# Kernel optimization log

Measured on AMD Instinct MI355X. Metric: run time of the kernel, lower is better.

The kernel has to match this reference:

```python
import jax, jax.numpy as jnp
import numpy as np

D = 256
H = 4
DH = D // H
DFF = 1024
EPS = 1e-5


def _split_heads(x):
    B, L, _ = x.shape
    return x.reshape(B, L, H, DH).transpose(0, 2, 1, 3)  # [B,H,L,dh]


def _merge_heads(o):
    B, h, L, dh = o.shape
    return o.transpose(0, 2, 1, 3).reshape(B, L, h * dh)


def _attention(Q, K, V, M):
    # Q,K,V: [B,H,Lq/Lk,dh]; M: [B,Lq,Lk] or [B,1,Lk]
    A = jnp.einsum('bhqd,bhkd->bhqk', Q, K) / (DH ** 0.5)
    A = jnp.where(M[:, None] == 0, -jnp.inf, A)
    A = jax.nn.softmax(A, axis=-1)
    return jnp.einsum('bhqk,bhkd->bhqd', A, V)


def _layernorm(x, g, b):
    mu = jnp.mean(x, axis=-1, keepdims=True)
    var = jnp.mean(jnp.square(x - mu), axis=-1, keepdims=True)
    return (x - mu) * jax.lax.rsqrt(var + EPS) * g + b


def setup_inputs() -> dict:
    key = jax.random.key(0)
    ks = jax.random.split(key, 14)
    B, T, S = 16, 1024, 1024
    s = 1.0 / (D ** 0.5)
    inp = {
        'X_target': jax.random.normal(ks[0], (B, T, D), jnp.float32),
        'outputMask': jnp.ones((B, T), jnp.float32),
        'X_encoder': jax.random.normal(ks[1], (B, S, D), jnp.float32),
        'inputMask': jnp.ones((B, S), jnp.float32),
        'Wq1': jax.random.normal(ks[2], (D, D), jnp.float32) * s,
        'Wk1': jax.random.normal(ks[3], (D, D), jnp.float32) * s,
        'Wv1': jax.random.normal(ks[4], (D, D), jnp.float32) * s,
        'Wo1': jax.random.normal(ks[5], (D, D), jnp.float32) * s,
        'Wq2': jax.random.normal(ks[6], (D, D), jnp.float32) * s,
        'Wk2': jax.random.normal(ks[7], (D, D), jnp.float32) * s,
        'Wv2': jax.random.normal(ks[8], (D, D), jnp.float32) * s,
        'Wo2': jax.random.normal(ks[9], (D, D), jnp.float32) * s,
        'W1': jax.random.normal(ks[10], (DFF, D), jnp.float32) * s,
        'W2': jax.random.normal(ks[11], (D, DFF), jnp.float32) * (1.0 / (DFF ** 0.5)),
        'g1': jnp.ones((D,), jnp.float32), 'b1': jnp.zeros((D,), jnp.float32),
        'g2': jnp.ones((D,), jnp.float32), 'b2': jnp.zeros((D,), jnp.float32),
        'g3': jnp.ones((D,), jnp.float32), 'b3': jnp.zeros((D,), jnp.float32),
    }
    return inp


def reference(X_target, outputMask, X_encoder, inputMask,
              Wq1, Wk1, Wv1, Wo1, Wq2, Wk2, Wv2, Wo2,
              W1, W2, g1, b1, g2, b2, g3, b3):
    T = X_target.shape[1]
    # combined causal * padding mask (intended tril of ones)
    tril = jnp.tril(jnp.ones((T, T), X_target.dtype))
    M_self = outputMask[:, None, :] * tril  # [B,T,T]
    M_cross = inputMask[:, None, :]         # [B,1,S]

    # masked self-attention (Linear: x @ W.T)
    Q = _split_heads(X_target @ Wq1.T)
    K = _split_heads(X_target @ Wk1.T)
    V = _split_heads(X_target @ Wv1.T)
    O = _merge_heads(_attention(Q, K, V, M_self)) @ Wo1.T
    X = X_target + _layernorm(O, g1, b1)  # AddNorm (dropout eval=identity)

    # cross-attention; note: output proj is O @ Wo2 (no transpose) in source
    Q = _split_heads(X @ Wq2.T)
    K = _split_heads(X_encoder @ Wk2.T)
    V = _split_heads(X_encoder @ Wv2.T)
    O = _merge_heads(_attention(Q, K, V, M_cross)) @ Wo2
    X = X + _layernorm(O, g2, b2)

    # FFN with ReLU after both linears (as in source)
    F = jax.nn.relu(jax.nn.relu(X @ W1.T) @ W2.T)
    X = X + _layernorm(F, g3, b3)
    return X
```

## Files before the change

### kernel.cpp

```cpp
#include <hip/hip_runtime.h>
#include <math.h>

#define D_ 256
#define H_ 4
#define DH_ 64
#define NKT_ 16
#define TPB_BITS 10

typedef __attribute__((ext_vector_type(8))) short bf16x8;
typedef __attribute__((ext_vector_type(4))) short short4v;
typedef __attribute__((ext_vector_type(4))) float f32x4;

__device__ __forceinline__ short f2bf(float x) {
  union { float f; unsigned u; } c; c.f = x;
  unsigned r = (c.u + 0x7fffu + ((c.u >> 16) & 1u)) >> 16;
  return (short)r;
}
__device__ __forceinline__ float bf2f(short s) {
  union { unsigned u; float f; } c; c.u = ((unsigned)(unsigned short)s) << 16;
  return c.f;
}
__device__ __forceinline__ unsigned cvtpk(float lo, float hi) {
  unsigned r;
  asm("v_cvt_pk_bf16_f32 %0, %1, %2" : "=v"(r) : "v"(lo), "v"(hi));
  return r;
}
#if __has_builtin(__builtin_amdgcn_exp2f)
#define EXP2F(x) __builtin_amdgcn_exp2f(x)
#else
#define EXP2F(x) __expf(0.6931471805599453f * (x))
#endif

__device__ __forceinline__ void gl_lds16(const void* g, void* lds) {
  __builtin_amdgcn_global_load_lds((const __attribute__((address_space(1))) void*)g,
                                   (__attribute__((address_space(3))) void*)lds,
                                   16, 0, 0);
}

template<bool ABF16, bool TRANSB, bool RELU, bool CBF16>
__global__ __launch_bounds__(256) void gemm_mfma(
    const void* __restrict__ A0, const void* __restrict__ A1, const void* __restrict__ A2,
    const float* __restrict__ B0, const float* __restrict__ B1, const float* __restrict__ B2,
    void* __restrict__ C0, void* __restrict__ C1, void* __restrict__ C2,
    int N, int K, int M, int vtrans_z, int ktile_z) {
  __shared__ short Al[2][128][72];
  __shared__ short Bl[2][128][72];
  const int tid = threadIdx.x;
  const int w   = tid >> 6;
  const int l   = tid & 63;
  const int bn  = blockIdx.x * 128;
  const int bm  = blockIdx.y * 128;
  const int z   = blockIdx.z;
  const void*  Av = (z == 0) ? A0 : ((z == 1) ? A1 : A2);
  const float* B  = (z == 0) ? B0 : ((z == 1) ? B1 : B2);
  void*        Cv = (z == 0) ? C0 : ((z == 1) ? C1 : C2);
  const int wm = (w >> 1) * 64;
  const int wn = (w & 1) * 64;
  const int fr = l & 15;
  const int fg = l >> 4;

  f32x4 acc[4][4];
  #pragma unroll
  for (int mi = 0; mi < 4; ++mi)
    #pragma unroll
    for (int ni = 0; ni < 4; ++ni) acc[mi][ni] = (f32x4){0.f, 0.f, 0.f, 0.f};

  const int sr = tid >> 1;
  const int sc = (tid & 1) * 32;

  float4 arf[8]; bf16x8 arb[4]; float4 brf[8];

  auto loadA = [&](int k0) {
    if (ABF16) {
      const short* arow = (const short*)Av + (size_t)(bn + sr) * K + k0 + sc;
      #pragma unroll
      for (int i = 0; i < 4; ++i) arb[i] = *(const bf16x8*)&arow[i * 8];
    } else {
      const float* arow = (const float*)Av + (size_t)(bn + sr) * K + k0 + sc;
      #pragma unroll
      for (int i = 0; i < 8; ++i) arf[i] = *(const float4*)&arow[i * 4];
    }
  };
  auto loadB = [&](int k0) {
    if (TRANSB) {
      const float* brow = B + (size_t)(bm + sr) * K + k0 + sc;
      #pragma unroll
      for (int i = 0; i < 8; ++i) brf[i] = *(const float4*)&brow[i * 4];
    } else {
      #pragma unroll
      for (int i = 0; i < 8; ++i) {
        int idx = tid + i * 256;
        int kk = idx >> 5;
        int c4 = (idx & 31) * 4;
        brf[i] = *(const float4*)&B[(size_t)(k0 + kk) * M + bm + c4];
      }
    }
  };
  auto store = [&](int buf) {
    if (ABF16) {
      #pragma unroll
      for (int i = 0; i < 4; ++i) *(bf16x8*)&Al[buf][sr][sc + i * 8] = arb[i];
    } else {
      #pragma unroll
      for (int i = 0; i < 8; ++i) {
        float4 v = arf[i];
        short4v s; s[0] = f2bf(v.x); s[1] = f2bf(v.y); s[2] = f2bf(v.z); s[3] = f2bf(v.w);
        *(short4v*)&Al[buf][sr][sc + i * 4] = s;
      }
    }
    if (TRANSB) {
      #pragma unroll
      for (int i = 0; i < 8; ++i) {
        float4 v = brf[i];
        short4v s; s[0] = f2bf(v.x); s[1] = f2bf(v.y); s[2] = f2bf(v.z); s[3] = f2bf(v.w);
        *(short4v*)&Bl[buf][sr][sc + i * 4] = s;
      }
    } else {
      #pragma unroll
      for (int i = 0; i < 8; ++i) {
        int idx = tid + i * 256;
        int kk = idx >> 5;
        int c4 = (idx & 31) * 4;
        float4 v = brf[i];
        Bl[buf][c4 + 0][kk] = f2bf(v.x);
        Bl[buf][c4 + 1][kk] = f2bf(v.y);
        Bl[buf][c4 + 2][kk] = f2bf(v.z);
        Bl[buf][c4 + 3][kk] = f2bf(v.w);
      }
    }
  };

  loadA(0); loadB(0); store(0);
  __syncthreads();
  const int nk = K >> 6;
  for (int s = 0; s < nk; ++s) {
    const int cur = s & 1;
    if (s + 1 < nk) { loadA((s + 1) << 6); loadB((s + 1) << 6); }
    #pragma unroll
    for (int kh = 0; kh < 2; ++kh) {
      bf16x8 af[4], bfr[4];
      #pragma unroll
      for (int mi = 0; mi < 4; ++mi)
        af[mi] = *(bf16x8*)&Al[cur][wm + mi * 16 + fr][kh * 32 + fg * 8];
      #pragma unroll
      for (int ni = 0; ni < 4; ++ni)
        bfr[ni] = *(bf16x8*)&Bl[cur][wn + ni * 16 + fr][kh * 32 + fg * 8];
      #pragma unroll
      for (int mi = 0; mi < 4; ++mi)
        #pragma unroll
        for (int ni = 0; ni < 4; ++ni)
          acc[mi][ni] = __builtin_amdgcn_mfma_f32_16x16x32_bf16(af[mi], bfr[ni], acc[mi][ni], 0, 0, 0);
    }
    if (s + 1 < nk) store(cur ^ 1);
    __syncthreads();
  }

  if (z == vtrans_z) {
    #pragma unroll
    for (int mi = 0; mi < 4; ++mi) {
      int nbase = bn + wm + mi * 16 + fg * 4;
      int b_  = nbase >> TPB_BITS;
      int key = nbase & ((1 << TPB_BITS) - 1);
      int kt  = key >> 6, kin = key & 63;
      #pragma unroll
      for (int ni = 0; ni < 4; ++ni) {
        int col = bm + wn + ni * 16 + fr;
        int h_ = col >> 6, dh = col & 63;
        short4v s;
        #pragma unroll
        for (int reg = 0; reg < 4; ++reg) s[reg] = f2bf(acc[mi][ni][reg]);
        size_t off = ((((size_t)(b_ * H_ + h_) * NKT_) + kt) << 12)
                   + dh * 64 + (((kin >> 3) ^ (dh & 7)) << 3) + (kin & 7);
        *(short4v*)&((short*)Cv)[off] = s;
      }
    }
  } else if (z == ktile_z) {
    #pragma unroll
    for (int mi = 0; mi < 4; ++mi) {
      #pragma unroll
      for (int reg = 0; reg < 4; ++reg) {
        int tok = bn + wm + mi * 16 + fg * 4 + reg;
        int b_  = tok >> TPB_BITS;
        int key = tok & ((1 << TPB_BITS) - 1);
        int kt  = key >> 6, kin = key & 63;
        size_t tb = ((((size_t)(b_ * H_) * NKT_) + kt) << 12) + kin * 64;
        #pragma unroll
        for (int ni = 0; ni < 4; ++ni) {
          int col = bm + wn + ni * 16 + fr;
          int h_ = col >> 6, dh = col & 63;
          size_t off = tb + (((size_t)h_ * NKT_) << 12)
                     + (((dh >> 3) ^ (kin & 7)) << 3) + (dh & 7);
          ((short*)Cv)[off] = f2bf(acc[mi][ni][reg]);
        }
      }
    }
  } else {
    #pragma unroll
    for (int mi = 0; mi < 4; ++mi) {
      #pragma unroll
      for (int reg = 0; reg < 4; ++reg) {
        size_t rowbase = (size_t)(bn + wm + mi * 16 + fg * 4 + reg) * M + bm + wn;
        #pragma unroll
        for (int ni = 0; ni < 4; ++ni) {
          float v = acc[mi][ni][reg];
          if (RELU) v = fmaxf(v, 0.f);
          if (CBF16) ((short*)Cv)[rowbase + ni * 16 + fr] = f2bf(v);
          else       ((float*)Cv)[rowbase + ni * 16 + fr] = v;
        }
      }
    }
  }
}

template<bool CAUSAL>
__global__ __launch_bounds__(256) void attn_mfma(const short* __restrict__ Q,
                                                 const short* __restrict__ KT,
                                                 const short* __restrict__ VT,
                                                 const float* __restrict__ mask,
                                                 short* __restrict__ O,
                                                 int T, int Lk) {
  constexpr int NS = CAUSAL ? 2 : 1;
  __shared__ short Kl[2][64][64];
  __shared__ short Vl[2][64][64];
  __shared__ short Pl[4][16][64];
  const int tid = threadIdx.x;
  const int l   = tid & 63;
  const int w   = tid >> 6;
  const int bh  = blockIdx.x;
  const int b   = bh >> 2;
  const int h   = bh & 3;
  const int r   = l & 15;
  const int g   = l >> 4;
  const float SCL2E = 0.125f * 1.4426950408889634f;

  const short* Ktile = KT + (((size_t)bh * (Lk >> 6)) << 12);
  const short* Vtile = VT + (((size_t)bh * (Lk >> 6)) << 12);
  const float* mrow  = mask + (size_t)b * Lk;

  int qt[NS];
  qt[0] = blockIdx.y;
  if (CAUSAL) qt[NS - 1] = (T >> 6) - 1 - blockIdx.y;
  const int nkt = CAUSAL ? (qt[NS - 1] + 1) : (Lk >> 6);

  bf16x8 qf[NS][2];
  #pragma unroll
  for (int s = 0; s < NS; ++s) {
    const short* qrow = Q + ((size_t)(b * T + qt[s] * 64 + w * 16 + r)) * D_ + h * DH_;
    qf[s][0] = *(const bf16x8*)&qrow[g * 8];
    qf[s][1] = *(const bf16x8*)&qrow[32 + g * 8];
  }

  float m[NS], ls[NS];
  f32x4 acc[NS][4];
  #pragma unroll
  for (int s = 0; s < NS; ++s) {
    m[s] = -1e30f; ls[s] = 0.f;
    #pragma unroll
    for (int dt = 0; dt < 4; ++dt) acc[s][dt] = (f32x4){0.f, 0.f, 0.f, 0.f};
  }

  auto stage = [&](int kt, int bb) {
    const short* ks = Ktile + ((size_t)kt << 12) + w * 1024 + (size_t)l * 8;
    const short* vs = Vtile + ((size_t)kt << 12) + w * 1024 + (size_t)l * 8;
    char* kd = (char*)&Kl[bb][0][0] + w * 2048;
    char* vd = (char*)&Vl[bb][0][0] + w * 2048;
    gl_lds16(ks,       kd);
    gl_lds16(ks + 512, kd + 1024);
    gl_lds16(vs,       vd);
    gl_lds16(vs + 512, vd + 1024);
  };

  stage(0, 0);
  __syncthreads();

  const int rx = r & 7;
  for (int kt = 0; kt < nkt; ++kt) {
    const int buf = kt & 1;
    if (kt + 1 < nkt) stage(kt + 1, buf ^ 1);

    const char* kb = (const char*)&Kl[buf][0][0];
    const char* vb = (const char*)&Vl[buf][0][0];

    f32x4 sfr[NS][4];
    #pragma unroll
    for (int s = 0; s < NS; ++s)
      #pragma unroll
      for (int st = 0; st < 4; ++st) sfr[s][st] = (f32x4){0.f, 0.f, 0.f, 0.f};
    __builtin_amdgcn_s_setprio(1);
    #pragma unroll
    for (int st = 0; st < 4; ++st) {
      #pragma unroll
      for (int kh = 0; kh < 2; ++kh) {
        bf16x8 kf = *(const bf16x8*)(kb + (st * 16 + r) * 128 + (((kh * 4 + g) ^ rx) << 4));
        #pragma unroll
        for (int s = 0; s < NS; ++s)
          if (!CAUSAL || kt <= qt[s])
            sfr[s][st] = __builtin_amdgcn_mfma_f32_16x16x32_bf16(kf, qf[s][kh], sfr[s][st], 0, 0, 0);
      }
    }
    __builtin_amdgcn_s_setprio(0);

    float mb[4][4];
    #pragma unroll
    for (int st = 0; st < 4; ++st) {
      float4 mv = *(const float4*)&mrow[kt * 64 + st * 16 + g * 4];
      #pragma unroll
      for (int reg = 0; reg < 4; ++reg)
        mb[st][reg] = fmaf((&mv.x)[reg], 1e30f, -1e30f);
    }

    #pragma unroll
    for (int s = 0; s < NS; ++s) {
      if (CAUSAL && kt > qt[s]) continue;
      float sc[4][4];
      #pragma unroll
      for (int st = 0; st < 4; ++st)
        #pragma unroll
        for (int reg = 0; reg < 4; ++reg)
          sc[st][reg] = fmaf(sfr[s][st][reg], SCL2E, mb[st][reg]);
      if (CAUSAL && kt == qt[s]) {
        #pragma unroll
        for (int st = 0; st < 4; ++st)
          #pragma unroll
          for (int reg = 0; reg < 4; ++reg)
            if (st * 16 + g * 4 + reg > w * 16 + r) sc[st][reg] = -1e30f;
      }

      float tm = sc[0][0];
      #pragma unroll
      for (int st = 0; st < 4; ++st)
        #pragma unroll
        for (int reg = 0; reg < 4; ++reg) tm = fmaxf(tm, sc[st][reg]);
      tm = fmaxf(tm, __shfl_xor(tm, 16));
      tm = fmaxf(tm, __shfl_xor(tm, 32));
      const int need = __any(tm - m[s] > 8.f);
      float mnew = need ? fmaxf(m[s], tm) : m[s];
      float pe[4][4], psum = 0.f;
      #pragma unroll
      for (int st = 0; st < 4; ++st)
        #pragma unroll
        for (int reg = 0; reg < 4; ++reg) {
          pe[st][reg] = EXP2F(sc[st][reg] - mnew);
          psum += pe[st][reg];
        }
      psum += __shfl_xor(psum, 16);
      psum += __shfl_xor(psum, 32);
      char* pw = (char*)&Pl[w][0][0] + r * 128;
      #pragma unroll
      for (int st = 0; st < 4; ++st) {
        uint2 u;
        u.x = cvtpk(pe[st][0], pe[st][1]);
        u.y = cvtpk(pe[st][2], pe[st][3]);
        *(uint2*)(pw + (((st * 2 + (g >> 1)) ^ rx) << 4) + (g & 1) * 8) = u;
      }
      if (need) {
        float alpha = EXP2F(m[s] - mnew);
        ls[s] = ls[s] * alpha + psum;
        m[s] = mnew;
        float af[4];
        #pragma unroll
        for (int reg = 0; reg < 4; ++reg) af[reg] = __shfl(alpha, g * 4 + reg);
        #pragma unroll
        for (int dt = 0; dt < 4; ++dt)
          #pragma unroll
          for (int reg = 0; reg < 4; ++reg) acc[s][dt][reg] *= af[reg];
      } else {
        ls[s] += psum;
      }

      __builtin_amdgcn_s_setprio(1);
      #pragma unroll
      for (int kh = 0; kh < 2; ++kh) {
        bf16x8 pf = *(const bf16x8*)((const char*)&Pl[w][0][0] + r * 128 + (((kh * 4 + g) ^ rx) << 4));
        #pragma unroll
        for (int dt = 0; dt < 4; ++dt) {
          bf16x8 vf = *(const bf16x8*)(vb + (dt * 16 + r) * 128 + (((kh * 4 + g) ^ rx) << 4));
          acc[s][dt] = __builtin_amdgcn_mfma_f32_16x16x32_bf16(pf, vf, acc[s][dt], 0, 0, 0);
        }
      }
      __builtin_amdgcn_s_setprio(0);
    }

    __syncthreads();
  }

  #pragma unroll
  for (int s = 0; s < NS; ++s) {
    float inv = (ls[s] > 0.f) ? (1.f / ls[s]) : 0.f;
    float invf[4];
    #pragma unroll
    for (int reg = 0; reg < 4; ++reg) invf[reg] = __shfl(inv, g * 4 + reg);
    #pragma unroll
    for (int reg = 0; reg < 4; ++reg) {
      short* orow = O + ((size_t)(b * T + qt[s] * 64 + w * 16 + g * 4 + reg)) * D_ + h * DH_;
      #pragma unroll
      for (int dt = 0; dt < 4; ++dt)
        orow[dt * 16 + r] = f2bf(acc[s][dt][reg] * invf[reg]);
    }
  }
}

template<bool RBF16, bool OBF16>
__global__ __launch_bounds__(256) void ln_res(const short* __restrict__ F,
                                              const void* __restrict__ Rv,
                                              const float* __restrict__ g,
                                              const float* __restrict__ bt,
                                              void* __restrict__ outv) {
  const int lane = threadIdx.x & 63;
  const int wid  = threadIdx.x >> 6;
  const size_t row  = (size_t)blockIdx.x * 4 + wid;
  const size_t base = row * 256 + (size_t)lane * 4;
  short4v fv = *(const short4v*)&F[base];
  float vx = bf2f(fv[0]), vy = bf2f(fv[1]), vz = bf2f(fv[2]), vw = bf2f(fv[3]);
  float s = vx + vy + vz + vw;
  #pragma unroll
  for (int o = 32; o >= 1; o >>= 1) s += __shfl_xor(s, o);
  float mu = s * (1.f / 256.f);
  float dx = vx - mu, dy = vy - mu, dz = vz - mu, dw = vw - mu;
  float vr = dx * dx + dy * dy + dz * dz + dw * dw;
  #pragma unroll
  for (int o = 32; o >= 1; o >>= 1) vr += __shfl_xor(vr, o);
  float rstd = rsqrtf(vr * (1.f / 256.f) + 1e-5f);
  float4 g4 = *(const float4*)&g[lane * 4];
  float4 b4 = *(const float4*)&bt[lane * 4];
  float rx, ry, rz, rw;
  if (RBF16) {
    short4v r4 = *(const short4v*)&((const short*)Rv)[base];
    rx = bf2f(r4[0]); ry = bf2f(r4[1]); rz = bf2f(r4[2]); rw = bf2f(r4[3]);
  } else {
    float4 r4 = *(const float4*)&((const float*)Rv)[base];
    rx = r4.x; ry = r4.y; rz = r4.z; rw = r4.w;
  }
  float ox = fmaf(dx * rstd, g4.x, b4.x) + rx;
  float oy = fmaf(dy * rstd, g4.y, b4.y) + ry;
  float oz = fmaf(dz * rstd, g4.z, b4.z) + rz;
  float ow = fmaf(dw * rstd, g4.w, b4.w) + rw;
  if (OBF16) {
    uint2 u; u.x = cvtpk(ox, oy); u.y = cvtpk(oz, ow);
    *(uint2*)&((short*)outv)[base] = u;
  } else {
    *(float4*)&((float*)outv)[base] = make_float4(ox, oy, oz, ow);
  }
}

extern "C" void kernel_launch(void* const* d_in, const int* in_sizes, int n_in,
                              void* d_out, int out_size, void* d_ws, size_t ws_size,
                              hipStream_t stream) {
  const float* Xt    = (const float*)d_in[0];
  const float* oMask = (const float*)d_in[1];
  const float* Xe    = (const float*)d_in[2];
  const float* iMask = (const float*)d_in[3];
  const float* Wq1   = (const float*)d_in[4];
  const float* Wk1   = (const float*)d_in[5];
  const float* Wv1   = (const float*)d_in[6];
  const float* Wo1   = (const float*)d_in[7];
  const float* Wq2   = (const float*)d_in[8];
  const float* Wk2   = (const float*)d_in[9];
  const float* Wv2   = (const float*)d_in[10];
  const float* Wo2   = (const float*)d_in[11];
  const float* W1    = (const float*)d_in[12];
  const float* W2    = (const float*)d_in[13];
  const float* g1    = (const float*)d_in[14];
  const float* b1    = (const float*)d_in[15];
  const float* g2    = (const float*)d_in[16];
  const float* b2    = (const float*)d_in[17];
  const float* g3    = (const float*)d_in[18];
  const float* b3    = (const float*)d_in[19];

  const int B = 16, T = 1024, S = 1024;
  const int NT = B * T;
  const size_t SZ = (size_t)NT * 256;

  float* ws = (float*)d_ws;
  float* s0 = ws;
  float* s1 = ws + SZ;
  float* s2 = ws + 2 * SZ;
  float* s3 = ws + 3 * SZ;
  float* s4 = ws + 4 * SZ;
  float* s5 = ws + 5 * SZ;
  short* b_s0 = (short*)s0; short* b_s1 = (short*)s1; short* b_s2 = (short*)s2;
  short* b_s3 = (short*)s3; short* b_s4 = (short*)s4; short* b_s5 = (short*)s5;

  dim3 blk(256);
  dim3 gQKV(NT / 128, 2, 3);
  dim3 gKV(NT / 128, 2, 2);
  dim3 gP1(NT / 128, 2, 1);
  dim3 gF1(NT / 128, 8, 1);
  dim3 gAs(B * H_, T / 128);
  dim3 gAc(B * H_, T / 64);

  gemm_mfma<false, true, false, true><<<gQKV, blk, 0, stream>>>(
      Xt, Xt, Xt, Wq1, Wk1, Wv1, s0, s1, s2, NT, 256, 256, 2, 1);
  attn_mfma<true><<<gAs, blk, 0, stream>>>(b_s0, b_s1, b_s2, oMask, b_s3, T, T);
  gemm_mfma<true, true, false, true><<<gP1, blk, 0, stream>>>(
      s3, s3, s3, Wo1, Wo1, Wo1, s0, s0, s0, NT, 256, 256, -1, -1);
  ln_res<false, true><<<NT / 4, blk, 0, stream>>>(b_s0, Xt, g1, b1, b_s4);

  gemm_mfma<true, true, false, true><<<gP1, blk, 0, stream>>>(
      s4, s4, s4, Wq2, Wq2, Wq2, s0, s0, s0, NT, 256, 256, -1, -1);
  gemm_mfma<false, true, false, true><<<gKV, blk, 0, stream>>>(
      Xe, Xe, Xe, Wk2, Wv2, Wv2, s1, s2, s2, NT, 256, 256, 1, 0);
  attn_mfma<false><<<gAc, blk, 0, stream>>>(b_s0, b_s1, b_s2, iMask, b_s3, T, S);
  gemm_mfma<true, false, false, true><<<gP1, blk, 0, stream>>>(
      s3, s3, s3, Wo2, Wo2, Wo2, s0, s0, s0, NT, 256, 256, -1, -1);
  ln_res<true, true><<<NT / 4, blk, 0, stream>>>(b_s0, b_s4, g2, b2, b_s5);

  gemm_mfma<true, true, true, true><<<gF1, blk, 0, stream>>>(
      s5, s5, s5, W1, W1, W1, s0, s0, s0, NT, 256, 1024, -1, -1);
  gemm_mfma<true, true, true, true><<<gP1, blk, 0, stream>>>(
      s0, s0, s0, W2, W2, W2, s4, s4, s4, NT, 1024, 256, -1, -1);
  ln_res<true, false><<<NT / 4, blk, 0, stream>>>(b_s4, b_s5, g3, b3, (float*)d_out);
}
```

Before: 245.5 us.

## Use 64-wide N tiles for narrow GEMMs and precompute mask bias

Templates the GEMM on the N-tile width and launches the 256-output GEMMs with 64-wide tiles, which doubles the grid and halves the per-block accumulators. The aim is better CU occupancy and more blocks in flight. A small pre-kernel turns the masks into additive bias arrays so the attention kernels no longer do the mask fmaf, and the row max is now a tree reduction. The cost is an extra launch and A tiles reloaded twice as often across blocks. The bias buffers are carved out of scratch space inside s3.

Measured after the change: 228.1 us. -7.1%, faster.

```diff
diff --git a/kernel.cpp b/kernel.cpp
--- a/kernel.cpp
+++ b/kernel.cpp
@@ -37,36 +37,51 @@
                                    16, 0, 0);
 }
 
-template<bool ABF16, bool TRANSB, bool RELU, bool CBF16>
+__global__ __launch_bounds__(256) void mask_bias(const float* __restrict__ m0,
+                                                 const float* __restrict__ m1,
+                                                 float* __restrict__ o0,
+                                                 float* __restrict__ o1, int n) {
+  int i = blockIdx.x * 256 + threadIdx.x;
+  if (i < n) {
+    o0[i] = (m0[i] != 0.f) ? 0.f : -1e30f;
+    o1[i] = (m1[i] != 0.f) ? 0.f : -1e30f;
+  }
+}
+
+template<int BN, bool ABF16, bool TRANSB, bool RELU, bool CBF16>
 __global__ __launch_bounds__(256) void gemm_mfma(
     const void* __restrict__ A0, const void* __restrict__ A1, const void* __restrict__ A2,
     const float* __restrict__ B0, const float* __restrict__ B1, const float* __restrict__ B2,
     void* __restrict__ C0, void* __restrict__ C1, void* __restrict__ C2,
     int N, int K, int M, int vtrans_z, int ktile_z) {
   __shared__ short Al[2][128][72];
-  __shared__ short Bl[2][128][72];
+  __shared__ short Bl[2][BN][72];
   const int tid = threadIdx.x;
   const int w   = tid >> 6;
   const int l   = tid & 63;
   const int bn  = blockIdx.x * 128;
-  const int bm  = blockIdx.y * 128;
+  const int bm  = blockIdx.y * BN;
   const int z   = blockIdx.z;
   const void*  Av = (z == 0) ? A0 : ((z == 1) ? A1 : A2);
   const float* B  = (z == 0) ? B0 : ((z == 1) ? B1 : B2);
   void*        Cv = (z == 0) ? C0 : ((z == 1) ? C1 : C2);
+  constexpr int NI = BN / 32;
   const int wm = (w >> 1) * 64;
-  const int wn = (w & 1) * 64;
+  const int wn = (w & 1) * (BN / 2);
   const int fr = l & 15;
   const int fg = l >> 4;
 
-  f32x4 acc[4][4];
+  f32x4 acc[4][NI];
   #pragma unroll
   for (int mi = 0; mi < 4; ++mi)
     #pragma unroll
-    for (int ni = 0; ni < 4; ++ni) acc[mi][ni] = (f32x4){0.f, 0.f, 0.f, 0.f};
+    for (int ni = 0; ni < NI; ++ni) acc[mi][ni] = (f32x4){0.f, 0.f, 0.f, 0.f};
 
   const int sr = tid >> 1;
   const int sc = (tid & 1) * 32;
+  constexpr int BRF = (BN == 128) ? 8 : 4;
+  const int brT = (BN == 128) ? (tid >> 1) : (tid >> 2);
+  const int bcT = (BN == 128) ? ((tid & 1) * 32) : ((tid & 3) * 16);
 
   float4 arf[8]; bf16x8 arb[4]; float4 brf[8];
 
@@ -83,15 +98,15 @@
   };
   auto loadB = [&](int k0) {
     if (TRANSB) {
-      const float* brow = B + (size_t)(bm + sr) * K + k0 + sc;
-      #pragma unroll
-      for (int i = 0; i < 8; ++i) brf[i] = *(const float4*)&brow[i * 4];
+      const float* brow = B + (size_t)(bm + brT) * K + k0 + bcT;
+      #pragma unroll
+      for (int i = 0; i < BRF; ++i) brf[i] = *(const float4*)&brow[i * 4];
     } else {
       #pragma unroll
-      for (int i = 0; i < 8; ++i) {
+      for (int i = 0; i < BRF; ++i) {
         int idx = tid + i * 256;
-        int kk = idx >> 5;
-        int c4 = (idx & 31) * 4;
+        int kk = (BN == 128) ? (idx >> 5) : (idx >> 4);
+        int c4 = (BN == 128) ? ((idx & 31) * 4) : ((idx & 15) * 4);
         brf[i] = *(const float4*)&B[(size_t)(k0 + kk) * M + bm + c4];
       }
     }
@@ -110,17 +125,17 @@
     }
     if (TRANSB) {
       #pragma unroll
-      for (int i = 0; i < 8; ++i) {
+      for (int i = 0; i < BRF; ++i) {
         float4 v = brf[i];
         short4v s; s[0] = f2bf(v.x); s[1] = f2bf(v.y); s[2] = f2bf(v.z); s[3] = f2bf(v.w);
-        *(short4v*)&Bl[buf][sr][sc + i * 4] = s;
+        *(short4v*)&Bl[buf][brT][bcT + i * 4] = s;
       }
     } else {
       #pragma unroll
-      for (int i = 0; i < 8; ++i) {
+      for (int i = 0; i < BRF; ++i) {
         int idx = tid + i * 256;
-        int kk = idx >> 5;
-        int c4 = (idx & 31) * 4;
+        int kk = (BN == 128) ? (idx >> 5) : (idx >> 4);
+        int c4 = (BN == 128) ? ((idx & 31) * 4) : ((idx & 15) * 4);
         float4 v = brf[i];
         Bl[buf][c4 + 0][kk] = f2bf(v.x);
         Bl[buf][c4 + 1][kk] = f2bf(v.y);
@@ -138,70 +153,76 @@
     if (s + 1 < nk) { loadA((s + 1) << 6); loadB((s + 1) << 6); }
     #pragma unroll
     for (int kh = 0; kh < 2; ++kh) {
-      bf16x8 af[4], bfr[4];
+      bf16x8 af[4], bfr[NI];
       #pragma unroll
       for (int mi = 0; mi < 4; ++mi)
         af[mi] = *(bf16x8*)&Al[cur][wm + mi * 16 + fr][kh * 32 + fg * 8];
       #pragma unroll
-      for (int ni = 0; ni < 4; ++ni)
+      for (int ni = 0; ni < NI; ++ni)
         bfr[ni] = *(bf16x8*)&Bl[cur][wn + ni * 16 + fr][kh * 32 + fg * 8];
       #pragma unroll
       for (int mi = 0; mi < 4; ++mi)
         #pragma unroll
-        for (int ni = 0; ni < 4; ++ni)
+        for (int ni = 0; ni < NI; ++ni)
           acc[mi][ni] = __builtin_amdgcn_mfma_f32_16x16x32_bf16(af[mi], bfr[ni], acc[mi][ni], 0, 0, 0);
     }
     if (s + 1 < nk) store(cur ^ 1);
     __syncthreads();
   }
 
-  if (z == vtrans_z) {
-    #pragma unroll
-    for (int mi = 0; mi < 4; ++mi) {
-      int nbase = bn + wm + mi * 16 + fg * 4;
-      int b_  = nbase >> TPB_BITS;
-      int key = nbase & ((1 << TPB_BITS) - 1);
-      int kt  = key >> 6, kin = key & 63;
-      #pragma unroll
-      for (int ni = 0; ni < 4; ++ni) {
-        int col = bm + wn + ni * 16 + fr;
-        int h_ = col >> 6, dh = col & 63;
-        short4v s;
-        #pragma unroll
-        for (int reg = 0; reg < 4; ++reg) s[reg] = f2bf(acc[mi][ni][reg]);
-        size_t off = ((((size_t)(b_ * H_ + h_) * NKT_) + kt) << 12)
-                   + dh * 64 + (((kin >> 3) ^ (dh & 7)) << 3) + (kin & 7);
-        *(short4v*)&((short*)Cv)[off] = s;
-      }
-    }
-  } else if (z == ktile_z) {
-    #pragma unroll
-    for (int mi = 0; mi < 4; ++mi) {
-      #pragma unroll
-      for (int reg = 0; reg < 4; ++reg) {
-        int tok = bn + wm + mi * 16 + fg * 4 + reg;
-        int b_  = tok >> TPB_BITS;
-        int key = tok & ((1 << TPB_BITS) - 1);
+  bool done = false;
+  if constexpr (BN == 128) {
+    if (z == vtrans_z) {
+      done = true;
+      #pragma unroll
+      for (int mi = 0; mi < 4; ++mi) {
+        int nbase = bn + wm + mi * 16 + fg * 4;
+        int b_  = nbase >> TPB_BITS;
+        int key = nbase & ((1 << TPB_BITS) - 1);
         int kt  = key >> 6, kin = key & 63;
-        size_t tb = ((((size_t)(b_ * H_) * NKT_) + kt) << 12) + kin * 64;
         #pragma unroll
         for (int ni = 0; ni < 4; ++ni) {
           int col = bm + wn + ni * 16 + fr;
           int h_ = col >> 6, dh = col & 63;
-          size_t off = tb + (((size_t)h_ * NKT_) << 12)
-                     + (((dh >> 3) ^ (kin & 7)) << 3) + (dh & 7);
-          ((short*)Cv)[off] = f2bf(acc[mi][ni][reg]);
+          short4v s;
+          #pragma unroll
+          for (int reg = 0; reg < 4; ++reg) s[reg] = f2bf(acc[mi][ni][reg]);
+          size_t off = ((((size_t)(b_ * H_ + h_) * NKT_) + kt) << 12)
+                     + dh * 64 + (((kin >> 3) ^ (dh & 7)) << 3) + (kin & 7);
+          *(short4v*)&((short*)Cv)[off] = s;
         }
       }
-    }
-  } else {
+    } else if (z == ktile_z) {
+      done = true;
+      #pragma unroll
+      for (int mi = 0; mi < 4; ++mi) {
+        #pragma unroll
+        for (int reg = 0; reg < 4; ++reg) {
+          int tok = bn + wm + mi * 16 + fg * 4 + reg;
+          int b_  = tok >> TPB_BITS;
+          int key = tok & ((1 << TPB_BITS) - 1);
+          int kt  = key >> 6, kin = key & 63;
+          size_t tb = ((((size_t)(b_ * H_) * NKT_) + kt) << 12) + kin * 64;
+          #pragma unroll
+          for (int ni = 0; ni < 4; ++ni) {
+            int col = bm + wn + ni * 16 + fr;
+            int h_ = col >> 6, dh = col & 63;
+            size_t off = tb + (((size_t)h_ * NKT_) << 12)
+                       + (((dh >> 3) ^ (kin & 7)) << 3) + (dh & 7);
+            ((short*)Cv)[off] = f2bf(acc[mi][ni][reg]);
+          }
+        }
+      }
+    }
+  }
+  if (!done) {
     #pragma unroll
     for (int mi = 0; mi < 4; ++mi) {
       #pragma unroll
       for (int reg = 0; reg < 4; ++reg) {
         size_t rowbase = (size_t)(bn + wm + mi * 16 + fg * 4 + reg) * M + bm + wn;
         #pragma unroll
-        for (int ni = 0; ni < 4; ++ni) {
+        for (int ni = 0; ni < NI; ++ni) {
           float v = acc[mi][ni][reg];
           if (RELU) v = fmaxf(v, 0.f);
           if (CBF16) ((short*)Cv)[rowbase + ni * 16 + fr] = f2bf(v);
@@ -216,7 +237,7 @@
 __global__ __launch_bounds__(256) void attn_mfma(const short* __restrict__ Q,
                                                  const short* __restrict__ KT,
                                                  const short* __restrict__ VT,
-                                                 const float* __restrict__ mask,
+                                                 const float* __restrict__ bias,
                                                  short* __restrict__ O,
                                                  int T, int Lk) {
   constexpr int NS = CAUSAL ? 2 : 1;
@@ -235,7 +256,7 @@
 
   const short* Ktile = KT + (((size_t)bh * (Lk >> 6)) << 12);
   const short* Vtile = VT + (((size_t)bh * (Lk >> 6)) << 12);
-  const float* mrow  = mask + (size_t)b * Lk;
+  const float* brow  = bias + (size_t)b * Lk;
 
   int qt[NS];
   qt[0] = blockIdx.y;
@@ -303,10 +324,8 @@
     float mb[4][4];
     #pragma unroll
     for (int st = 0; st < 4; ++st) {
-      float4 mv = *(const float4*)&mrow[kt * 64 + st * 16 + g * 4];
-      #pragma unroll
-      for (int reg = 0; reg < 4; ++reg)
-        mb[st][reg] = fmaf((&mv.x)[reg], 1e30f, -1e30f);
+      float4 mv = *(const float4*)&brow[kt * 64 + st * 16 + g * 4];
+      mb[st][0] = mv.x; mb[st][1] = mv.y; mb[st][2] = mv.z; mb[st][3] = mv.w;
     }
 
     #pragma unroll
@@ -326,11 +345,12 @@
             if (st * 16 + g * 4 + reg > w * 16 + r) sc[st][reg] = -1e30f;
       }
 
-      float tm = sc[0][0];
-      #pragma unroll
-      for (int st = 0; st < 4; ++st)
-        #pragma unroll
-        for (int reg = 0; reg < 4; ++reg) tm = fmaxf(tm, sc[st][reg]);
+      float t0 = fmaxf(fmaxf(sc[0][0], sc[0][1]), sc[0][2]);
+      float t1 = fmaxf(fmaxf(sc[0][3], sc[1][0]), sc[1][1]);
+      float t2 = fmaxf(fmaxf(sc[1][2], sc[1][3]), sc[2][0]);
+      float t3 = fmaxf(fmaxf(sc[2][1], sc[2][2]), sc[2][3]);
+      float t4 = fmaxf(fmaxf(sc[3][0], sc[3][1]), sc[3][2]);
+      float tm = fmaxf(fmaxf(fmaxf(t0, t1), fmaxf(t2, t3)), fmaxf(t4, sc[3][3]));
       tm = fmaxf(tm, __shfl_xor(tm, 16));
       tm = fmaxf(tm, __shfl_xor(tm, 32));
       const int need = __any(tm - m[s] > 8.f);
@@ -480,34 +500,38 @@
   float* s5 = ws + 5 * SZ;
   short* b_s0 = (short*)s0; short* b_s1 = (short*)s1; short* b_s2 = (short*)s2;
   short* b_s3 = (short*)s3; short* b_s4 = (short*)s4; short* b_s5 = (short*)s5;
+  float* biasS = s3 + 3 * (SZ / 4);
+  float* biasC = biasS + B * S;
 
   dim3 blk(256);
   dim3 gQKV(NT / 128, 2, 3);
   dim3 gKV(NT / 128, 2, 2);
-  dim3 gP1(NT / 128, 2, 1);
+  dim3 gS64(NT / 128, 4, 1);
   dim3 gF1(NT / 128, 8, 1);
   dim3 gAs(B * H_, T / 128);
   dim3 gAc(B * H_, T / 64);
 
-  gemm_mfma<false, true, false, true><<<gQKV, blk, 0, stream>>>(
+  mask_bias<<<64, blk, 0, stream>>>(oMask, iMask, biasS, biasC, B * T);
+
+  gemm_mfma<128, false, true, false, true><<<gQKV, blk, 0, stream>>>(
       Xt, Xt, Xt, Wq1, Wk1, Wv1, s0, s1, s2, NT, 256, 256, 2, 1);
-  attn_mfma<true><<<gAs, blk, 0, stream>>>(b_s0, b_s1, b_s2, oMask, b_s3, T, T);
-  gemm_mfma<true, true, false, true><<<gP1, blk, 0, stream>>>(
+  attn_mfma<true><<<gAs, blk, 0, stream>>>(b_s0, b_s1, b_s2, biasS, b_s3, T, T);
+  gemm_mfma<64, true, true, false, true><<<gS64, blk, 0, stream>>>(
       s3, s3, s3, Wo1, Wo1, Wo1, s0, s0, s0, NT, 256, 256, -1, -1);
   ln_res<false, true><<<NT / 4, blk, 0, stream>>>(b_s0, Xt, g1, b1, b_s4);
 
-  gemm_mfma<true, true, false, true><<<gP1, blk, 0, stream>>>(
+  gemm_mfma<64, true, true, false, true><<<gS64, blk, 0, stream>>>(
       s4, s4, s4, Wq2, Wq2, Wq2, s0, s0, s0, NT, 256, 256, -1, -1);
-  gemm_mfma<false, true, false, true><<<gKV, blk, 0, stream>>>(
+  gemm_mfma<128, false, true, false, true><<<gKV, blk, 0, stream>>>(
       Xe, Xe, Xe, Wk2, Wv2, Wv2, s1, s2, s2, NT, 256, 256, 1, 0);
-  attn_mfma<false><<<gAc, blk, 0, stream>>>(b_s0, b_s1, b_s2, iMask, b_s3, T, S);
-  gemm_mfma<true, false, false, true><<<gP1, blk, 0, stream>>>(
+  attn_mfma<false><<<gAc, blk, 0, stream>>>(b_s0, b_s1, b_s2, biasC, b_s3, T, S);
+  gemm_mfma<64, true, false, false, true><<<gS64, blk, 0, stream>>>(
       s3, s3, s3, Wo2, Wo2, Wo2, s0, s0, s0, NT, 256, 256, -1, -1);
   ln_res<true, true><<<NT / 4, blk, 0, stream>>>(b_s0, b_s4, g2, b2, b_s5);
 
-  gemm_mfma<true, true, true, true><<<gF1, blk, 0, stream>>>(
+  gemm_mfma<128, true, true, true, true><<<gF1, blk, 0, stream>>>(
       s5, s5, s5, W1, W1, W1, s0, s0, s0, NT, 256, 1024, -1, -1);
-  gemm_mfma<true, true, true, true><<<gP1, blk, 0, stream>>>(
+  gemm_mfma<64, true, true, true, true><<<gS64, blk, 0, stream>>>(
       s0, s0, s0, W2, W2, W2, s4, s4, s4, NT, 1024, 256, -1, -1);
   ln_res<true, false><<<NT / 4, blk, 0, stream>>>(b_s4, b_s5, g3, b3, (float*)d_out);
 }
```
